# Kernel tuning notes

Hardware: AMD Instinct MI355X
Metric: run time of the kernel (lower is better)

Reference implementation:

```python
import jax, jax.numpy as jnp
import numpy as np

N_EMBD = 768
N_HEAD = 12
HEAD_DIM = N_EMBD // N_HEAD


def setup_inputs() -> dict:
    key = jax.random.key(0)
    ks = jax.random.split(key, 5)
    B, S = 4, 2048
    x = jax.random.normal(ks[0], (B, S, N_EMBD), dtype=jnp.float32)
    scale = 0.02
    w_attn = jax.random.normal(ks[1], (N_EMBD, 3 * N_EMBD), dtype=jnp.float32) * scale
    b_attn = jnp.zeros((3 * N_EMBD,), dtype=jnp.float32)
    w_proj = jax.random.normal(ks[2], (N_EMBD, N_EMBD), dtype=jnp.float32) * scale
    b_proj = jnp.zeros((N_EMBD,), dtype=jnp.float32)
    return {"x": x, "w_attn": w_attn, "b_attn": b_attn, "w_proj": w_proj, "b_proj": b_proj}


def reference(x, w_attn, b_attn, w_proj, b_proj):
    B, S, E = x.shape
    qkv = x @ w_attn + b_attn  # [B,S,3E]
    q, k, v = jnp.split(qkv, 3, axis=2)
    # [B,H,S,D]
    q = q.reshape(B, S, N_HEAD, HEAD_DIM).transpose(0, 2, 1, 3)
    k = k.reshape(B, S, N_HEAD, HEAD_DIM).transpose(0, 2, 1, 3)
    v = v.reshape(B, S, N_HEAD, HEAD_DIM).transpose(0, 2, 1, 3)
    scores = jnp.einsum('bhqd,bhkd->bhqk', q, k) / jnp.sqrt(jnp.float32(HEAD_DIM))
    causal = jnp.tril(jnp.ones((S, S), dtype=bool))
    scores = jnp.where(causal[None, None], scores, jnp.float32(-jnp.inf))
    weights = jax.nn.softmax(scores, axis=-1)
    out = jnp.einsum('bhqk,bhkd->bhqd', weights, v)
    out = out.transpose(0, 2, 1, 3).reshape(B, S, E)
    return out @ w_proj + b_proj
```

## Files before the change

### kernel.cpp

```cpp
#include <hip/hip_runtime.h>
#include <hip/hip_bf16.h>

typedef __attribute__((ext_vector_type(8))) __bf16 bf16x8;
typedef __attribute__((ext_vector_type(4))) __bf16 bf16x4;
typedef __attribute__((ext_vector_type(4))) float f32x4;

#define E_ 768
#define HEADS 12
#define HD 64
#define S_ 2048
#define B_ 4

__device__ inline unsigned short f2bf(float f) {
    union { float f; unsigned int u; } x{f};
    unsigned int r = x.u + 0x7FFFu + ((x.u >> 16) & 1u);
    return (unsigned short)(r >> 16);
}

__global__ void cvt_kernel(const float* __restrict__ in, unsigned short* __restrict__ out, int n4) {
    int i = blockIdx.x * blockDim.x + threadIdx.x;
    if (i < n4) {
        float4 v = reinterpret_cast<const float4*>(in)[i];
        ushort4 o;
        o.x = f2bf(v.x); o.y = f2bf(v.y); o.z = f2bf(v.z); o.w = f2bf(v.w);
        reinterpret_cast<ushort4*>(out)[i] = o;
    }
}

__global__ void transpose_cvt(const float* __restrict__ w, unsigned short* __restrict__ wT,
                              int K, int N) {
    __shared__ float tile[32][33];
    int n0 = blockIdx.x * 32, k0 = blockIdx.y * 32;
    int tx = threadIdx.x, ty = threadIdx.y;
    tile[ty][tx] = w[(size_t)(k0 + ty) * N + n0 + tx];
    __syncthreads();
    wT[(size_t)(n0 + ty) * K + k0 + tx] = f2bf(tile[tx][ty]);
}

template<int MODE>
__global__ __launch_bounds__(256) void gemm16(
    const unsigned short* __restrict__ A, const unsigned short* __restrict__ Bt,
    const float* __restrict__ bias,
    unsigned short* __restrict__ Qo, unsigned short* __restrict__ Ko,
    unsigned short* __restrict__ Vt, float* __restrict__ Of,
    int M, int N, int K)
{
    __shared__ unsigned short Sh[128 * 128];
    unsigned short* Ash = Sh;
    unsigned short* Bsh = Sh + 128 * 64;

    const int nbx = N >> 7;
    const int nwg = (M >> 7) * nbx;
    const int cpx = nwg >> 3;
    const int orig = blockIdx.x;
    const int wgid = (orig & 7) * cpx + (orig >> 3);
    const int row0 = (wgid / nbx) * 128;
    const int col0 = (wgid % nbx) * 128;

    const int t = threadIdx.x;
    const int w = t >> 6, lane = t & 63;
    const int lr = lane & 15, lc = lane >> 4;
    const int wrow = (w >> 1) * 64;
    const int wcol = (w & 1) * 64;

    const int srow = lane >> 3;
    const int sslot = lane & 7;

    f32x4 acc[4][4] = {};

    for (int k0 = 0; k0 < K; k0 += 64) {
#pragma unroll
        for (int j = 0; j < 4; j++) {
            const int rbase = j * 32 + w * 8;
            const unsigned short* ga = A + (size_t)(row0 + rbase + srow) * K + k0 + sslot * 8;
            __builtin_amdgcn_global_load_lds(
                (const __attribute__((address_space(1))) void*)ga,
                (__attribute__((address_space(3))) void*)&Ash[rbase * 64], 16, 0, 0);
            const unsigned short* gb = Bt + (size_t)(col0 + rbase + srow) * K + k0 + sslot * 8;
            __builtin_amdgcn_global_load_lds(
                (const __attribute__((address_space(1))) void*)gb,
                (__attribute__((address_space(3))) void*)&Bsh[rbase * 64], 16, 0, 0);
        }
        __syncthreads();

#pragma unroll
        for (int ks = 0; ks < 2; ks++) {
            bf16x8 a[4], b[4];
#pragma unroll
            for (int i = 0; i < 4; i++)
                a[i] = *reinterpret_cast<const bf16x8*>(&Ash[(wrow + i * 16 + lr) * 64 + ks * 32 + lc * 8]);
#pragma unroll
            for (int j2 = 0; j2 < 4; j2++)
                b[j2] = *reinterpret_cast<const bf16x8*>(&Bsh[(wcol + j2 * 16 + lr) * 64 + ks * 32 + lc * 8]);
#pragma unroll
            for (int i = 0; i < 4; i++)
#pragma unroll
                for (int j2 = 0; j2 < 4; j2++)
                    acc[i][j2] = __builtin_amdgcn_mfma_f32_16x16x32_bf16(a[i], b[j2], acc[i][j2], 0, 0, 0);
        }
        __syncthreads();
    }

    if constexpr (MODE == 0) {
        if (col0 >= 2 * E_) {
#pragma unroll
            for (int i = 0; i < 4; i++)
#pragma unroll
                for (int j = 0; j < 4; j++) {
                    const int c = wcol + j * 16 + lr;
                    const float bv = bias[col0 + c];
#pragma unroll
                    for (int r = 0; r < 4; r++) {
                        const int row = wrow + i * 16 + lc * 4 + r;
                        Sh[c * 128 + (row ^ ((c & 15) << 3))] = f2bf(acc[i][j][r] + bv);
                    }
                }
            __syncthreads();
            const int bb = row0 >> 11;
            const int s0 = row0 & (S_ - 1);
            const int nnb = col0 - 2 * E_;
#pragma unroll
            for (int pass = 0; pass < 8; pass++) {
                const int c = pass * 16 + (t >> 4);
                const int sL = (t & 15) * 8;
                bf16x8 vv = *reinterpret_cast<const bf16x8*>(&Sh[c * 128 + (sL ^ ((c & 15) << 3))]);
                const int h = (nnb + c) >> 6, d = c & 63;
                const size_t bh = (size_t)(bb * HEADS + h);
                *reinterpret_cast<bf16x8*>(&Vt[(bh * HD + d) * S_ + s0 + sL]) = vv;
            }
            return;
        }
#pragma unroll
        for (int i = 0; i < 4; i++)
#pragma unroll
            for (int j = 0; j < 4; j++) {
                int col = col0 + wcol + j * 16 + lr;
                float bv = bias[col];
#pragma unroll
                for (int r = 0; r < 4; r++) {
                    int row = row0 + wrow + i * 16 + lc * 4 + r;
                    float val = acc[i][j][r] + bv;
                    int bb = row >> 11, s = row & (S_ - 1);
                    int which = col / E_;
                    int nn = col - which * E_;
                    int h = nn >> 6, d = nn & 63;
                    size_t bh = (size_t)(bb * HEADS + h);
                    if (which == 0)      Qo[(bh * S_ + s) * HD + d] = f2bf(val * 0.125f);
                    else                 Ko[(bh * S_ + s) * HD + d] = f2bf(val);
                }
            }
    } else {
#pragma unroll
        for (int i = 0; i < 4; i++)
#pragma unroll
            for (int j = 0; j < 4; j++) {
                int col = col0 + wcol + j * 16 + lr;
                float bv = bias[col];
#pragma unroll
                for (int r = 0; r < 4; r++) {
                    int row = row0 + wrow + i * 16 + lc * 4 + r;
                    Of[(size_t)row * N + col] = acc[i][j][r] + bv;
                }
            }
    }
}

__global__ __launch_bounds__(256) void attn_kernel(
    const unsigned short* __restrict__ Q, const unsigned short* __restrict__ Kd,
    const unsigned short* __restrict__ Vt, unsigned short* __restrict__ O)
{
    __shared__ unsigned short Ksh[128 * 64];
    __shared__ unsigned short Vsh[64 * 128];
    __shared__ unsigned short Pl[4][16 * 128];

    const int t = threadIdx.x;
    const int w = t >> 6, lane = t & 63;
    const int lr = lane & 15, lc = lane >> 4;
    const int g = blockIdx.x;
    const int bp = g / 48;
    const int bh = g - bp * 48;
    const int tTL = bp, tTH = 31 - bp;
    const int qLrow0 = tTL * 64 + w * 16;
    const int qHrow0 = tTH * 64 + w * 16;
    const int nL = (tTL + 2) >> 1;

    const unsigned short* Qb = Q + (size_t)bh * S_ * HD;
    const unsigned short* Kb = Kd + (size_t)bh * S_ * HD;
    const unsigned short* Vb = Vt + (size_t)bh * HD * S_;

    const int srK = t >> 3, ssK = t & 7;
    const int kws = ((ssK ^ (srK & 7)) << 3);
    const int srV = t >> 4, ssV = t & 15;
    const int vws = ((ssV ^ (srV & 15)) << 3);
    const int r7 = lr & 7;

    const unsigned short* KbS = Kb + (size_t)srK * HD + ssK * 8;
    const unsigned short* VbS = Vb + (size_t)srV * S_ + ssV * 8;

    bf16x8 aqL[2], aqH[2];
#pragma unroll
    for (int dc = 0; dc < 2; dc++) {
        aqL[dc] = *reinterpret_cast<const bf16x8*>(Qb + (size_t)(qLrow0 + lr) * HD + dc * 32 + lc * 8);
        aqH[dc] = *reinterpret_cast<const bf16x8*>(Qb + (size_t)(qHrow0 + lr) * HD + dc * 32 + lc * 8);
    }

    f32x4 o[4] = {};
    float m = -INFINITY, l = 0.f;

    int bb = bh / HEADS, hh = bh - bb * HEADS;

    bf16x8 kreg[4], vreg[4];
#pragma unroll
    for (int i = 0; i < 4; i++) {
        kreg[i] = *reinterpret_cast<const bf16x8*>(KbS + i * 32 * HD);
        vreg[i] = *reinterpret_cast<const bf16x8*>(VbS + i * 16 * S_);
    }

    bf16x8 aq0 = aqL[0], aq1 = aqL[1];
    int qrow = qLrow0 + lr;

    for (int it = 0; it < 17; ++it) {
        __syncthreads();
#pragma unroll
        for (int i = 0; i < 4; i++) {
            *reinterpret_cast<bf16x8*>(&Ksh[(srK + i * 32) * 64 + kws]) = kreg[i];
            *reinterpret_cast<bf16x8*>(&Vsh[(srV + i * 16) * 128 + vws]) = vreg[i];
        }
        __syncthreads();

        if (it + 1 < 17) {
            const int nkv0 = (it + 1 < nL) ? (it + 1) * 128 : (it + 1 - nL) * 128;
#pragma unroll
            for (int i = 0; i < 4; i++) {
                kreg[i] = *reinterpret_cast<const bf16x8*>(KbS + (size_t)nkv0 * HD + i * 32 * HD);
                vreg[i] = *reinterpret_cast<const bf16x8*>(VbS + nkv0 + i * 16 * S_);
            }
        }

        if (it == nL) {
            float lq[4];
#pragma unroll
            for (int r = 0; r < 4; r++) lq[r] = __shfl(l, lc * 4 + r);
#pragma unroll
            for (int r = 0; r < 4; r++) {
                float inv = 1.f / lq[r];
                int qr = qLrow0 + lc * 4 + r;
#pragma unroll
                for (int dt = 0; dt < 4; dt++)
                    O[((size_t)(bb * S_ + qr)) * E_ + hh * HD + dt * 16 + lr] = f2bf(o[dt][r] * inv);
            }
            m = -INFINITY; l = 0.f;
#pragma unroll
            for (int dt = 0; dt < 4; dt++)
#pragma unroll
                for (int r = 0; r < 4; r++) o[dt][r] = 0.f;
            aq0 = aqH[0]; aq1 = aqH[1];
            qrow = qHrow0 + lr;
        }

        const int kv0 = (it < nL) ? it * 128 : (it - nL) * 128;
        const bool needMask = (it == nL - 1) || (it == 16);

        float p[8][4];
#pragma unroll
        for (int kt = 0; kt < 8; kt++) {
            const int row = kt * 16 + lr;
            const bf16x8 bk0 = *reinterpret_cast<const bf16x8*>(&Ksh[row * 64 + ((lc ^ r7) << 3)]);
            const bf16x8 bk1 = *reinterpret_cast<const bf16x8*>(&Ksh[row * 64 + (((4 + lc) ^ r7) << 3)]);
            f32x4 s = {};
            s = __builtin_amdgcn_mfma_f32_16x16x32_bf16(bk0, aq0, s, 0, 0, 0);
            s = __builtin_amdgcn_mfma_f32_16x16x32_bf16(bk1, aq1, s, 0, 0, 0);
#pragma unroll
            for (int r = 0; r < 4; r++) p[kt][r] = s[r];
        }
        if (needMask) {
#pragma unroll
            for (int kt = 0; kt < 8; kt++) {
                const int kbase = kv0 + kt * 16 + lc * 4;
#pragma unroll
                for (int r = 0; r < 4; r++)
                    if (kbase + r > qrow) p[kt][r] = -1e30f;
            }
        }

        float rm = -1e30f;
#pragma unroll
        for (int kt = 0; kt < 8; kt++)
#pragma unroll
            for (int r = 0; r < 4; r++) rm = fmaxf(rm, p[kt][r]);
        rm = fmaxf(rm, __shfl_xor(rm, 16));
        rm = fmaxf(rm, __shfl_xor(rm, 32));

        const bool grow = !__all(rm <= m);
        float mn = m, sc;
        if (grow) {
            mn = fmaxf(m, rm);
            sc = __expf(m - mn);
        }

        float rs = 0.f;
#pragma unroll
        for (int kt = 0; kt < 8; kt++)
#pragma unroll
            for (int r = 0; r < 4; r++) {
                float e = __expf(p[kt][r] - mn);
                p[kt][r] = e; rs += e;
            }
        rs += __shfl_xor(rs, 16);
        rs += __shfl_xor(rs, 32);

        if (grow) {
            l = l * sc + rs;
            m = mn;
            float scq[4];
#pragma unroll
            for (int r = 0; r < 4; r++) scq[r] = __shfl(sc, lc * 4 + r);
#pragma unroll
            for (int dt = 0; dt < 4; dt++)
#pragma unroll
                for (int r = 0; r < 4; r++) o[dt][r] *= scq[r];
        } else {
            l += rs;
        }

#pragma unroll
        for (int kt = 0; kt < 8; kt++) {
            bf16x4 pv4;
            pv4[0] = (__bf16)p[kt][0]; pv4[1] = (__bf16)p[kt][1];
            pv4[2] = (__bf16)p[kt][2]; pv4[3] = (__bf16)p[kt][3];
            const int phys = (2 * kt + (lc >> 1)) ^ r7;
            *reinterpret_cast<bf16x4*>(&Pl[w][lr * 128 + phys * 8 + (lc & 1) * 4]) = pv4;
        }
        asm volatile("s_waitcnt lgkmcnt(0)" ::: "memory");
        __builtin_amdgcn_sched_barrier(0);

        bf16x8 ap[4];
#pragma unroll
        for (int kc = 0; kc < 4; kc++)
            ap[kc] = *reinterpret_cast<const bf16x8*>(&Pl[w][lr * 128 + (((kc * 4 + lc) ^ r7) << 3)]);

#pragma unroll
        for (int dt = 0; dt < 4; dt++) {
            const int row = dt * 16 + lr;
#pragma unroll
            for (int kc = 0; kc < 4; kc++) {
                const bf16x8 bv = *reinterpret_cast<const bf16x8*>(
                    &Vsh[row * 128 + (((kc * 4 + lc) ^ lr) << 3)]);
                o[dt] = __builtin_amdgcn_mfma_f32_16x16x32_bf16(ap[kc], bv, o[dt], 0, 0, 0);
            }
        }
    }

    {
        float lq[4];
#pragma unroll
        for (int r = 0; r < 4; r++) lq[r] = __shfl(l, lc * 4 + r);
#pragma unroll
        for (int r = 0; r < 4; r++) {
            float inv = 1.f / lq[r];
            int qr = qHrow0 + lc * 4 + r;
#pragma unroll
            for (int dt = 0; dt < 4; dt++)
                O[((size_t)(bb * S_ + qr)) * E_ + hh * HD + dt * 16 + lr] = f2bf(o[dt][r] * inv);
        }
    }
}

extern "C" void kernel_launch(void* const* d_in, const int* in_sizes, int n_in,
                              void* d_out, int out_size, void* d_ws, size_t ws_size,
                              hipStream_t stream) {
    const float* x      = (const float*)d_in[0];
    const float* w_attn = (const float*)d_in[1];
    const float* b_attn = (const float*)d_in[2];
    const float* w_proj = (const float*)d_in[3];
    const float* b_proj = (const float*)d_in[4];
    float* out = (float*)d_out;

    char* ws = (char*)d_ws;
    const size_t M = (size_t)B_ * S_;
    unsigned short* xb  = (unsigned short*)(ws);
    unsigned short* waT = (unsigned short*)(ws + 12582912);
    unsigned short* wpT = (unsigned short*)(ws + 16121856);
    unsigned short* Qb  = (unsigned short*)(ws + 17301504);
    unsigned short* Kb  = (unsigned short*)(ws + 29884416);
    unsigned short* Vt  = (unsigned short*)(ws + 42467328);
    unsigned short* AO  = (unsigned short*)(ws + 55050240);

    int n4 = (int)(M * E_ / 4);
    cvt_kernel<<<(n4 + 255) / 256, 256, 0, stream>>>(x, xb, n4);
    transpose_cvt<<<dim3(3 * E_ / 32, E_ / 32), dim3(32, 32), 0, stream>>>(w_attn, waT, E_, 3 * E_);
    transpose_cvt<<<dim3(E_ / 32, E_ / 32), dim3(32, 32), 0, stream>>>(w_proj, wpT, E_, E_);

    gemm16<0><<<1152, 256, 0, stream>>>(
        xb, waT, b_attn, Qb, Kb, Vt, nullptr, (int)M, 3 * E_, E_);

    attn_kernel<<<768, 256, 0, stream>>>(Qb, Kb, Vt, AO);

    gemm16<1><<<384, 256, 0, stream>>>(
        AO, wpT, b_proj, nullptr, nullptr, nullptr, out, (int)M, E_, E_);
}
```

Measured before the change: 168.4 us.

## Feed softmax probabilities to PV MFMA from registers by permuting V layout

```diff
diff --git a/kernel.cpp b/kernel.cpp
--- a/kernel.cpp
+++ b/kernel.cpp
@@ -171,7 +171,6 @@
 {
     __shared__ unsigned short Ksh[128 * 64];
     __shared__ unsigned short Vsh[64 * 128];
-    __shared__ unsigned short Pl[4][16 * 128];
 
     const int t = threadIdx.x;
     const int w = t >> 6, lane = t & 63;
@@ -191,7 +190,10 @@
     const int srK = t >> 3, ssK = t & 7;
     const int kws = ((ssK ^ (srK & 7)) << 3);
     const int srV = t >> 4, ssV = t & 15;
-    const int vws = ((ssV ^ (srV & 15)) << 3);
+    const int vs1 = (ssV >> 2) * 4 + (ssV & 1) * 2;
+    const int voff = ((ssV >> 1) & 1) * 4;
+    const int vws1 = ((vs1 ^ srV) << 3) + voff;
+    const int vws2 = (((vs1 + 1) ^ srV) << 3) + voff;
     const int r7 = lr & 7;
 
     const unsigned short* KbS = Kb + (size_t)srK * HD + ssK * 8;
@@ -224,7 +226,11 @@
 #pragma unroll
         for (int i = 0; i < 4; i++) {
             *reinterpret_cast<bf16x8*>(&Ksh[(srK + i * 32) * 64 + kws]) = kreg[i];
-            *reinterpret_cast<bf16x8*>(&Vsh[(srV + i * 16) * 128 + vws]) = vreg[i];
+            union { bf16x8 v; bf16x4 h[2]; } u;
+            u.v = vreg[i];
+            const int vrow = (srV + i * 16) * 128;
+            *reinterpret_cast<bf16x4*>(&Vsh[vrow + vws1]) = u.h[0];
+            *reinterpret_cast<bf16x4*>(&Vsh[vrow + vws2]) = u.h[1];
         }
         __syncthreads();
 
@@ -323,21 +329,16 @@
             l += rs;
         }
 
-#pragma unroll
-        for (int kt = 0; kt < 8; kt++) {
-            bf16x4 pv4;
-            pv4[0] = (__bf16)p[kt][0]; pv4[1] = (__bf16)p[kt][1];
-            pv4[2] = (__bf16)p[kt][2]; pv4[3] = (__bf16)p[kt][3];
-            const int phys = (2 * kt + (lc >> 1)) ^ r7;
-            *reinterpret_cast<bf16x4*>(&Pl[w][lr * 128 + phys * 8 + (lc & 1) * 4]) = pv4;
-        }
-        asm volatile("s_waitcnt lgkmcnt(0)" ::: "memory");
-        __builtin_amdgcn_sched_barrier(0);
-
         bf16x8 ap[4];
 #pragma unroll
-        for (int kc = 0; kc < 4; kc++)
-            ap[kc] = *reinterpret_cast<const bf16x8*>(&Pl[w][lr * 128 + (((kc * 4 + lc) ^ r7) << 3)]);
+        for (int kc = 0; kc < 4; kc++) {
+            union { bf16x8 v; __bf16 b[8]; } u;
+            u.b[0] = (__bf16)p[2 * kc][0];     u.b[1] = (__bf16)p[2 * kc][1];
+            u.b[2] = (__bf16)p[2 * kc][2];     u.b[3] = (__bf16)p[2 * kc][3];
+            u.b[4] = (__bf16)p[2 * kc + 1][0]; u.b[5] = (__bf16)p[2 * kc + 1][1];
+            u.b[6] = (__bf16)p[2 * kc + 1][2]; u.b[7] = (__bf16)p[2 * kc + 1][3];
+            ap[kc] = u.v;
+        }
 
 #pragma unroll
         for (int dt = 0; dt < 4; dt++) {
```

Result: faster. 164.1 us (-2.5%).
